# Kernel tuning notes

Hardware: AMD Instinct MI355X
Metric: run time of the kernel (lower is better)

## Reference

```python
import jax, jax.numpy as jnp
import numpy as np

INPUT_SIZE = 1024
HIDDEN = 2048
B = 4096


def setup_inputs() -> dict:
    key = jax.random.key(0)
    ks = jax.random.split(key, 11)
    D = INPUT_SIZE + HIDDEN
    bound = 1.0 / np.sqrt(D)  # nn.Linear default init range
    def lin(kw, kb):
        W = jax.random.uniform(kw, (HIDDEN, D), jnp.float32, -bound, bound)
        b = jax.random.uniform(kb, (HIDDEN,), jnp.float32, -bound, bound)
        return W, b
    W_i, b_i = lin(ks[0], ks[1])
    W_f, b_f = lin(ks[2], ks[3])
    W_c, b_c = lin(ks[4], ks[5])
    W_o, b_o = lin(ks[6], ks[7])
    x_t = jax.random.normal(ks[8], (B, INPUT_SIZE), jnp.float32)
    h_prev = jax.random.normal(ks[9], (B, HIDDEN), jnp.float32)
    c_prev = jax.random.normal(ks[10], (B, HIDDEN), jnp.float32)
    return {
        "x_t": x_t, "h_prev": h_prev, "c_prev": c_prev,
        "W_i": W_i, "b_i": b_i, "W_f": W_f, "b_f": b_f,
        "W_c": W_c, "b_c": b_c, "W_o": W_o, "b_o": b_o,
    }


def reference(x_t, h_prev, c_prev, W_i, b_i, W_f, b_f, W_c, b_c, W_o, b_o):
    # combined: [B, input+hidden]
    combined = jnp.concatenate([x_t, h_prev], axis=1)
    # fused gate GEMM: stack the four weight matrices -> one [D, 4H] matmul
    W_all = jnp.concatenate([W_i, W_f, W_c, W_o], axis=0)  # [4H, D]
    b_all = jnp.concatenate([b_i, b_f, b_c, b_o], axis=0)  # [4H]
    gates = combined @ W_all.T + b_all                     # [B, 4H]
    gi, gf, gc, go = jnp.split(gates, 4, axis=1)
    i_t = jax.nn.sigmoid(gi)
    f_t = jax.nn.sigmoid(gf)
    g_t = jnp.tanh(gc)
    o_t = jax.nn.sigmoid(go)
    c_t = f_t * c_prev + i_t * g_t
    h_t = o_t * jnp.tanh(c_t)
    # dropout is identity in eval / p=0
    return (h_t, c_t)
```

## Files before the change

### kernel.cpp

```cpp
#include <hip/hip_runtime.h>
#include <stdint.h>

#define B_DIM 4096
#define IN_SZ 1024
#define HID   2048
#define D_DIM 3072
#define BM 128
#define BH 32
#define BK 32

typedef float  f32x4  __attribute__((ext_vector_type(4)));
typedef short  short8 __attribute__((ext_vector_type(8)));

__device__ __forceinline__ unsigned short f2bf(float f) {
    union { float f; unsigned u; } v; v.f = f;
    unsigned u = v.u + 0x7fffu + ((v.u >> 16) & 1u);
    return (unsigned short)(u >> 16);
}

__device__ __forceinline__ void async_load16(const void* g, void* l) {
    __builtin_amdgcn_global_load_lds(
        (const __attribute__((address_space(1))) unsigned int*)g,
        (__attribute__((address_space(3))) unsigned int*)l,
        16, 0, 0);
}

__device__ __forceinline__ float sigm(float x) {
    return 1.0f / (1.0f + __expf(-x));
}
__device__ __forceinline__ float tanh_f(float x) {
    return 1.0f - 2.0f / (__expf(2.0f * x) + 1.0f);
}

__global__ void convert_combined(const float* __restrict__ x,
                                 const float* __restrict__ h,
                                 unsigned short* __restrict__ dst) {
    int idx = blockIdx.x * blockDim.x + threadIdx.x;
    const int C4 = D_DIM / 4;
    if (idx >= B_DIM * C4) return;
    int b  = idx / C4;
    int c4 = idx - b * C4;
    float4 v;
    if (c4 < IN_SZ / 4) v = ((const float4*)x)[b * (IN_SZ / 4) + c4];
    else                v = ((const float4*)h)[b * (HID / 4) + (c4 - IN_SZ / 4)];
    ushort4 o;
    o.x = f2bf(v.x); o.y = f2bf(v.y); o.z = f2bf(v.z); o.w = f2bf(v.w);
    ((ushort4*)dst)[idx] = o;
}

__global__ void convert_W(const float* __restrict__ W0, const float* __restrict__ W1,
                          const float* __restrict__ W2, const float* __restrict__ W3,
                          unsigned short* __restrict__ dst) {
    int idx = blockIdx.x * blockDim.x + threadIdx.x;
    const int PG = HID * D_DIM / 4;
    if (idx >= 4 * PG) return;
    int g = idx / PG;
    int r = idx - g * PG;
    const float* W = (g == 0) ? W0 : (g == 1) ? W1 : (g == 2) ? W2 : W3;
    float4 v = ((const float4*)W)[r];
    ushort4 o;
    o.x = f2bf(v.x); o.y = f2bf(v.y); o.z = f2bf(v.z); o.w = f2bf(v.w);
    ((ushort4*)dst)[idx] = o;
}

__global__ __launch_bounds__(256, 2)
void lstm_gemm(const unsigned short* __restrict__ Abf,
               const unsigned short* __restrict__ Wbf,
               const float* __restrict__ b_i, const float* __restrict__ b_f,
               const float* __restrict__ b_c, const float* __restrict__ b_o,
               const float* __restrict__ c_prev,
               float* __restrict__ h_out, float* __restrict__ c_out) {
    __shared__ unsigned short sA[BM * BK];
    __shared__ unsigned short sB[BM * BK];

    const int tid  = threadIdx.x;
    const int lane = tid & 63;
    const int wave = tid >> 6;
    const int l16  = lane & 15;
    const int quad = lane >> 4;

    const int m0 = blockIdx.x * BM;
    const int h0 = blockIdx.y * BH;

    f32x4 acc[2][8] = {};

    const int srow = lane >> 2;
    const int scol = (lane & 3) * 8;
    const unsigned short* gA = Abf + (size_t)(m0 + wave * 32 + srow) * D_DIM + scol;
    const unsigned short* gB = Wbf + (size_t)(wave * HID + h0 + srow) * D_DIM + scol;
    unsigned short* lA0 = &sA[(wave * 32) * BK];
    unsigned short* lA1 = &sA[(wave * 32 + 16) * BK];
    unsigned short* lB0 = &sB[(wave * 32) * BK];
    unsigned short* lB1 = &sB[(wave * 32 + 16) * BK];

    for (int kk = 0; kk < D_DIM / BK; ++kk) {
        const int k0 = kk * BK;
        if (kk) __syncthreads();
        async_load16(gA + k0,                 lA0 + lane * 8);
        async_load16(gA + 16 * D_DIM + k0,    lA1 + lane * 8);
        async_load16(gB + k0,                 lB0 + lane * 8);
        async_load16(gB + 16 * D_DIM + k0,    lB1 + lane * 8);
        __syncthreads();

        short8 a0 = *(const short8*)&sA[(wave * 32 + l16) * BK + quad * 8];
        short8 a1 = *(const short8*)&sA[(wave * 32 + 16 + l16) * BK + quad * 8];
#pragma unroll
        for (int ct = 0; ct < 8; ++ct) {
            short8 b = *(const short8*)&sB[(ct * 16 + l16) * BK + quad * 8];
            acc[0][ct] = __builtin_amdgcn_mfma_f32_16x16x32_bf16(a0, b, acc[0][ct], 0, 0, 0);
            acc[1][ct] = __builtin_amdgcn_mfma_f32_16x16x32_bf16(a1, b, acc[1][ct], 0, 0, 0);
        }
    }

    const int rbase = m0 + wave * 32 + quad * 4;
#pragma unroll
    for (int cj = 0; cj < 2; ++cj) {
        const int h  = h0 + cj * 16 + l16;
        const float bi = b_i[h], bf = b_f[h], bc = b_c[h], bo = b_o[h];
#pragma unroll
        for (int rt = 0; rt < 2; ++rt) {
#pragma unroll
            for (int r = 0; r < 4; ++r) {
                const int m = rbase + rt * 16 + r;
                const size_t off = (size_t)m * HID + h;
                float gi = acc[rt][0 + cj][r] + bi;
                float gf = acc[rt][2 + cj][r] + bf;
                float gc = acc[rt][4 + cj][r] + bc;
                float go = acc[rt][6 + cj][r] + bo;
                float it = sigm(gi);
                float ft = sigm(gf);
                float gt = tanh_f(gc);
                float ot = sigm(go);
                float c  = ft * c_prev[off] + it * gt;
                float hv = ot * tanh_f(c);
                h_out[off] = hv;
                c_out[off] = c;
            }
        }
    }
}

extern "C" void kernel_launch(void* const* d_in, const int* in_sizes, int n_in,
                              void* d_out, int out_size, void* d_ws, size_t ws_size,
                              hipStream_t stream) {
    const float* x_t    = (const float*)d_in[0];
    const float* h_prev = (const float*)d_in[1];
    const float* c_prev = (const float*)d_in[2];
    const float* W_i = (const float*)d_in[3];
    const float* b_i = (const float*)d_in[4];
    const float* W_f = (const float*)d_in[5];
    const float* b_f = (const float*)d_in[6];
    const float* W_c = (const float*)d_in[7];
    const float* b_c = (const float*)d_in[8];
    const float* W_o = (const float*)d_in[9];
    const float* b_o = (const float*)d_in[10];
    float* out = (float*)d_out;

    unsigned short* Abf = (unsigned short*)d_ws;
    unsigned short* Wbf = (unsigned short*)((char*)d_ws + (size_t)B_DIM * D_DIM * 2);

    {
        int n = B_DIM * D_DIM / 4;
        convert_combined<<<(n + 255) / 256, 256, 0, stream>>>(x_t, h_prev, Abf);
    }
    {
        int n = 4 * HID * D_DIM / 4;
        convert_W<<<(n + 255) / 256, 256, 0, stream>>>(W_i, W_f, W_c, W_o, Wbf);
    }
    dim3 grid(B_DIM / BM, HID / BH);
    lstm_gemm<<<grid, 256, 0, stream>>>(Abf, Wbf, b_i, b_f, b_c, b_o, c_prev,
                                        out, out + (size_t)B_DIM * HID);
}
```

Measured before the change: 463.5 us.

## Double M tile to 256 rows and use lane-major LDS layout

New measurement: 498.9 us. 7.6% more time.

```diff
diff --git a/kernel.cpp b/kernel.cpp
--- a/kernel.cpp
+++ b/kernel.cpp
@@ -5,7 +5,7 @@
 #define IN_SZ 1024
 #define HID   2048
 #define D_DIM 3072
-#define BM 128
+#define BM 256
 #define BH 32
 #define BK 32
 
@@ -71,7 +71,7 @@
                const float* __restrict__ c_prev,
                float* __restrict__ h_out, float* __restrict__ c_out) {
     __shared__ unsigned short sA[BM * BK];
-    __shared__ unsigned short sB[BM * BK];
+    __shared__ unsigned short sB[4 * BH * BK];
 
     const int tid  = threadIdx.x;
     const int lane = tid & 63;
@@ -82,43 +82,46 @@
     const int m0 = blockIdx.x * BM;
     const int h0 = blockIdx.y * BH;
 
-    f32x4 acc[2][8] = {};
+    f32x4 acc[4][8] = {};
 
-    const int srow = lane >> 2;
-    const int scol = (lane & 3) * 8;
-    const unsigned short* gA = Abf + (size_t)(m0 + wave * 32 + srow) * D_DIM + scol;
+    const int srow = lane & 15;
+    const int scol = (lane >> 4) * 8;
+    const unsigned short* gA = Abf + (size_t)(m0 + wave * 64 + srow) * D_DIM + scol;
     const unsigned short* gB = Wbf + (size_t)(wave * HID + h0 + srow) * D_DIM + scol;
-    unsigned short* lA0 = &sA[(wave * 32) * BK];
-    unsigned short* lA1 = &sA[(wave * 32 + 16) * BK];
-    unsigned short* lB0 = &sB[(wave * 32) * BK];
-    unsigned short* lB1 = &sB[(wave * 32 + 16) * BK];
+    unsigned short* lA = &sA[(wave * 4) * 512];
+    unsigned short* lB = &sB[(wave * 2) * 512];
 
     for (int kk = 0; kk < D_DIM / BK; ++kk) {
         const int k0 = kk * BK;
         if (kk) __syncthreads();
-        async_load16(gA + k0,                 lA0 + lane * 8);
-        async_load16(gA + 16 * D_DIM + k0,    lA1 + lane * 8);
-        async_load16(gB + k0,                 lB0 + lane * 8);
-        async_load16(gB + 16 * D_DIM + k0,    lB1 + lane * 8);
+        async_load16(gA + 0 * 16 * D_DIM + k0, lA + 0 * 512);
+        async_load16(gA + 1 * 16 * D_DIM + k0, lA + 1 * 512);
+        async_load16(gA + 2 * 16 * D_DIM + k0, lA + 2 * 512);
+        async_load16(gA + 3 * 16 * D_DIM + k0, lA + 3 * 512);
+        async_load16(gB + 0 * 16 * D_DIM + k0, lB + 0 * 512);
+        async_load16(gB + 1 * 16 * D_DIM + k0, lB + 1 * 512);
         __syncthreads();
 
-        short8 a0 = *(const short8*)&sA[(wave * 32 + l16) * BK + quad * 8];
-        short8 a1 = *(const short8*)&sA[(wave * 32 + 16 + l16) * BK + quad * 8];
+        short8 a[4];
+#pragma unroll
+        for (int rt = 0; rt < 4; ++rt)
+            a[rt] = *(const short8*)&sA[(wave * 4 + rt) * 512 + quad * 128 + l16 * 8];
 #pragma unroll
         for (int ct = 0; ct < 8; ++ct) {
-            short8 b = *(const short8*)&sB[(ct * 16 + l16) * BK + quad * 8];
-            acc[0][ct] = __builtin_amdgcn_mfma_f32_16x16x32_bf16(a0, b, acc[0][ct], 0, 0, 0);
-            acc[1][ct] = __builtin_amdgcn_mfma_f32_16x16x32_bf16(a1, b, acc[1][ct], 0, 0, 0);
+            short8 b = *(const short8*)&sB[ct * 512 + quad * 128 + l16 * 8];
+#pragma unroll
+            for (int rt = 0; rt < 4; ++rt)
+                acc[rt][ct] = __builtin_amdgcn_mfma_f32_16x16x32_bf16(a[rt], b, acc[rt][ct], 0, 0, 0);
         }
     }
 
-    const int rbase = m0 + wave * 32 + quad * 4;
+    const int rbase = m0 + wave * 64 + quad * 4;
 #pragma unroll
     for (int cj = 0; cj < 2; ++cj) {
         const int h  = h0 + cj * 16 + l16;
         const float bi = b_i[h], bf = b_f[h], bc = b_c[h], bo = b_o[h];
 #pragma unroll
-        for (int rt = 0; rt < 2; ++rt) {
+        for (int rt = 0; rt < 4; ++rt) {
 #pragma unroll
             for (int r = 0; r < 4; ++r) {
                 const int m = rbase + rt * 16 + r;
```
